# Optimization experiments

Measured on AMD Instinct MI355X. Metric: run time of the kernel, lower is better.

Reference implementation:

```python
import jax, jax.numpy as jnp
import numpy as np

B, S = 4, 2000            # meshes, nodes per mesh
N = B * S                  # total nodes
E = 32000                  # directed edges (before self loops)
H_TR, D_TR, FF, TOUT = 4, 64, 2048, 16
HID, HEADS, HC = 512, 6, 512
DEFORM_IN, NUM_LOOP = 7, 3


def setup_inputs():
    key = jax.random.key(0)
    ks = iter(jax.random.split(key, 64))
    def W(shape):
        return jax.random.normal(next(ks), shape, jnp.float32) / np.sqrt(shape[-1])
    inp = {}
    inp['conv_feat'] = jax.random.normal(next(ks), (B, 1), jnp.float32)
    inp['mesh_feat'] = jax.random.normal(next(ks), (N, 4), jnp.float32)
    inp['x'] = jax.random.normal(next(ks), (N, DEFORM_IN), jnp.float32)
    inp['edge_index'] = jax.random.randint(next(ks), (2, E), 0, N, jnp.int32)
    inp['embed_w'] = W((D_TR, 4)); inp['embed_b'] = jnp.zeros((D_TR,), jnp.float32)
    inp['in_proj_w'] = W((3 * D_TR, D_TR)); inp['in_proj_b'] = jnp.zeros((3 * D_TR,), jnp.float32)
    inp['out_proj_w'] = W((D_TR, D_TR)); inp['out_proj_b'] = jnp.zeros((D_TR,), jnp.float32)
    inp['ln1_g'] = jnp.ones((D_TR,), jnp.float32); inp['ln1_b'] = jnp.zeros((D_TR,), jnp.float32)
    inp['ln2_g'] = jnp.ones((D_TR,), jnp.float32); inp['ln2_b'] = jnp.zeros((D_TR,), jnp.float32)
    inp['ff1_w'] = W((FF, D_TR)); inp['ff1_b'] = jnp.zeros((FF,), jnp.float32)
    inp['ff2_w'] = W((D_TR, FF)); inp['ff2_b'] = jnp.zeros((D_TR,), jnp.float32)
    inp['tout_w'] = W((TOUT, D_TR)); inp['tout_b'] = jnp.zeros((TOUT,), jnp.float32)
    all_feat = DEFORM_IN - 2 + TOUT  # 21
    inp['lin_w'] = W((HID, all_feat)); inp['lin_b'] = jnp.zeros((HID,), jnp.float32)
    gin = 2 + HID  # 514
    inp['gat_wl'] = W((HEADS * HC, gin)); inp['gat_bl'] = jnp.zeros((HEADS * HC,), jnp.float32)
    inp['gat_wr'] = W((HEADS * HC, gin)); inp['gat_br'] = jnp.zeros((HEADS * HC,), jnp.float32)
    inp['gat_att'] = jax.random.normal(next(ks), (HEADS, HC), jnp.float32) / np.sqrt(HC)
    inp['gat_bias'] = jnp.zeros((HC,), jnp.float32)
    inp['coord1_w'] = W((HID // 2, HID)); inp['coord1_b'] = jnp.zeros((HID // 2,), jnp.float32)
    inp['coord2_w'] = W((2, HID // 2)); inp['coord2_b'] = jnp.zeros((2,), jnp.float32)
    return inp


def _ln(h, g, b):
    m = jnp.mean(h, -1, keepdims=True)
    v = jnp.var(h, -1, keepdims=True)
    return (h - m) / jnp.sqrt(v + 1e-5) * g + b


def _mrt_forward(conv_feat, mesh_feat, x, edge_index, embed_w, embed_b, in_proj_w, in_proj_b,
                 out_proj_w, out_proj_b, ln1_g, ln1_b, ln2_g, ln2_b, ff1_w, ff1_b, ff2_w, ff2_b,
                 tout_w, tout_b, lin_w, lin_b, gat_wl, gat_bl, gat_wr, gat_br, gat_att, gat_bias,
                 coord1_w, coord1_b, coord2_w, coord2_b):
    bsz = conv_feat.shape[0]
    feat_dim = mesh_feat.shape[-1]
    # ---- transformer encoder (1 post-norm layer, eval mode => no dropout) ----
    h = mesh_feat.reshape(bsz, -1, feat_dim) @ embed_w.T + embed_b  # [B,S,D]
    qkv = h @ in_proj_w.T + in_proj_b
    q, k, v = jnp.split(qkv, 3, axis=-1)
    dh = D_TR // H_TR
    hd = lambda t: t.reshape(bsz, -1, H_TR, dh)
    attn = jax.nn.softmax(jnp.einsum('bqhd,bkhd->bhqk', hd(q), hd(k)) / np.sqrt(dh), axis=-1)
    o = jnp.einsum('bhqk,bkhd->bqhd', attn, hd(v)).reshape(bsz, -1, D_TR)
    h = _ln(h + (o @ out_proj_w.T + out_proj_b), ln1_g, ln1_b)
    ff = jax.nn.relu(h @ ff1_w.T + ff1_b) @ ff2_w.T + ff2_b
    h = _ln(h + ff, ln2_g, ln2_b)
    feats = (h @ tout_w.T + tout_b).reshape(-1, TOUT)               # [N,16]
    feats = jnp.concatenate([x[:, 2:], feats], axis=1)             # [N,21]
    hidden = jax.nn.selu(feats @ lin_w.T + lin_b)                  # [N,512]
    # ---- recurrent GATv2 deformer loop ----
    coord = x[:, :2]
    n = x.shape[0]
    loops = jnp.arange(n, dtype=edge_index.dtype)                  # self loops (GATv2Conv default)
    src = jnp.concatenate([edge_index[0], loops])
    dst = jnp.concatenate([edge_index[1], loops])
    for _ in range(NUM_LOOP):
        inp = jnp.concatenate([coord, hidden], axis=1)             # [N,514]
        xl = (inp @ gat_wl.T + gat_bl).reshape(n, HEADS, HC)
        xr = (inp @ gat_wr.T + gat_br).reshape(n, HEADS, HC)
        e = jax.nn.leaky_relu(xl[src] + xr[dst], 0.2)              # [Etot,H,C]
        logits = jnp.einsum('ehc,hc->eh', e, gat_att)              # [Etot,H]
        mx = jax.ops.segment_max(logits, dst, num_segments=n)
        a = jnp.exp(logits - mx[dst])
        a = a / jax.ops.segment_sum(a, dst, num_segments=n)[dst]   # softmax per dst node
        agg = jax.ops.segment_sum(xl[src] * a[:, :, None], dst, num_segments=n)  # [N,H,C]
        hidden = jax.nn.selu(jnp.mean(agg, axis=1) + gat_bias)     # concat=False => head mean
        coord = jax.nn.selu(hidden @ coord1_w.T + coord1_b) @ coord2_w.T + coord2_b
    return coord


def reference(conv_feat, mesh_feat, x, edge_index, embed_w, embed_b, in_proj_w, in_proj_b,
              out_proj_w, out_proj_b, ln1_g, ln1_b, ln2_g, ln2_b, ff1_w, ff1_b, ff2_w, ff2_b,
              tout_w, tout_b, lin_w, lin_b, gat_wl, gat_bl, gat_wr, gat_br, gat_att, gat_bias,
              coord1_w, coord1_b, coord2_w, coord2_b):
    return _mrt_forward(conv_feat, mesh_feat, x, edge_index, embed_w, embed_b, in_proj_w, in_proj_b,
                        out_proj_w, out_proj_b, ln1_g, ln1_b, ln2_g, ln2_b, ff1_w, ff1_b, ff2_w, ff2_b,
                        tout_w, tout_b, lin_w, lin_b, gat_wl, gat_bl, gat_wr, gat_br, gat_att, gat_bias,
                        coord1_w, coord1_b, coord2_w, coord2_b)
```

## Files before the change

kernel.cpp:

```cpp
#include <hip/hip_runtime.h>
#include <hip/hip_bf16.h>
#include <math.h>

#define NN     8000
#define MPAD   8064
#define BATCH  4
#define SEQ    2000
#define DTR    64
#define NHTR   4
#define DHD    16
#define FFD    2048
#define TOUTD  16
#define HIDD   512
#define NHEADS 6
#define HCD    512
#define GIND   514
#define GOUT   3072
#define GOUT2  6144
#define NEDGE  32000
#define ELOOP  40000

#define K1     576
#define K2     1152

#define KSPLIT 20
#define KCH    100

#define CDIV(a,b) (((a)+(b)-1)/(b))

using bf16x8 = __attribute__((__ext_vector_type__(8))) __bf16;
using f32x4  = __attribute__((__ext_vector_type__(4))) float;

__device__ __forceinline__ float selu_f(float x){
  const float a = 1.6732632423543772848f;
  const float s = 1.0507009873554805f;
  return x > 0.f ? s * x : s * a * (__expf(x) - 1.f);
}

__device__ __forceinline__ unsigned short f2bf_rn(float x){
  unsigned u = __float_as_uint(x);
  unsigned r = (u + 0x7fffu + ((u >> 16) & 1u)) >> 16;
  return (unsigned short)r;
}
__device__ __forceinline__ float bf2f(unsigned short h){
  return __uint_as_float((unsigned)h << 16);
}

template<int ACT>
__global__ __launch_bounds__(256) void k_gemm(const float* __restrict__ A,
    const float* __restrict__ W, const float* __restrict__ bias,
    float* __restrict__ C, int M, int N, int K)
{
  __shared__ float As[16][68];
  __shared__ float Ws[16][68];
  const int tid = threadIdx.x;
  const int bm = blockIdx.y * 64, bn = blockIdx.x * 64;
  const int tx = tid & 15, ty = tid >> 4;
  float acc[4][4] = {};
  for (int k0 = 0; k0 < K; k0 += 16){
    #pragma unroll
    for (int i = 0; i < 4; ++i){
      int el = tid + (i << 8);
      int kk = el & 15, r = el >> 4;
      int gk = k0 + kk;
      int gm = bm + r;
      As[kk][r] = (gm < M && gk < K) ? A[(size_t)gm * K + gk] : 0.f;
      int gn = bn + r;
      Ws[kk][r] = (gn < N && gk < K) ? W[(size_t)gn * K + gk] : 0.f;
    }
    __syncthreads();
    #pragma unroll
    for (int kk = 0; kk < 16; ++kk){
      float av[4], wv[4];
      #pragma unroll
      for (int i = 0; i < 4; ++i) av[i] = As[kk][ty*4+i];
      #pragma unroll
      for (int j = 0; j < 4; ++j) wv[j] = Ws[kk][tx*4+j];
      #pragma unroll
      for (int i = 0; i < 4; ++i)
        #pragma unroll
        for (int j = 0; j < 4; ++j) acc[i][j] = fmaf(av[i], wv[j], acc[i][j]);
    }
    __syncthreads();
  }
  #pragma unroll
  for (int i = 0; i < 4; ++i){
    int gm = bm + ty*4 + i;
    if (gm >= M) continue;
    #pragma unroll
    for (int j = 0; j < 4; ++j){
      int gn = bn + tx*4 + j;
      if (gn >= N) continue;
      float v = acc[i][j] + bias[gn];
      if (ACT == 1) v = fmaxf(v, 0.f);
      if (ACT == 2) v = selu_f(v);
      C[(size_t)gm * N + gn] = v;
    }
  }
}

__global__ __launch_bounds__(256) void k_gemm_sk(const float* __restrict__ A,
    const float* __restrict__ W, float* __restrict__ part,
    int M, int N, int K, int kchunk)
{
  __shared__ float As[16][68];
  __shared__ float Ws[16][68];
  const int tid = threadIdx.x;
  const int bm = blockIdx.y * 64, bn = blockIdx.x * 64;
  const int kbeg = blockIdx.z * kchunk;
  const int tx = tid & 15, ty = tid >> 4;
  float acc[4][4] = {};
  for (int k0 = kbeg; k0 < kbeg + kchunk; k0 += 16){
    #pragma unroll
    for (int i = 0; i < 4; ++i){
      int el = tid + (i << 8);
      int kk = el & 15, r = el >> 4;
      int gk = k0 + kk;
      int gm = bm + r;
      As[kk][r] = (gm < M && gk < K) ? A[(size_t)gm * K + gk] : 0.f;
      int gn = bn + r;
      Ws[kk][r] = (gn < N && gk < K) ? W[(size_t)gn * K + gk] : 0.f;
    }
    __syncthreads();
    #pragma unroll
    for (int kk = 0; kk < 16; ++kk){
      float av[4], wv[4];
      #pragma unroll
      for (int i = 0; i < 4; ++i) av[i] = As[kk][ty*4+i];
      #pragma unroll
      for (int j = 0; j < 4; ++j) wv[j] = Ws[kk][tx*4+j];
      #pragma unroll
      for (int i = 0; i < 4; ++i)
        #pragma unroll
        for (int j = 0; j < 4; ++j) acc[i][j] = fmaf(av[i], wv[j], acc[i][j]);
    }
    __syncthreads();
  }
  float* pz = part + (size_t)blockIdx.z * M * N;
  #pragma unroll
  for (int i = 0; i < 4; ++i){
    int gm = bm + ty*4 + i;
    if (gm >= M) continue;
    #pragma unroll
    for (int j = 0; j < 4; ++j){
      int gn = bn + tx*4 + j;
      if (gn >= N) continue;
      pz[(size_t)gm * N + gn] = acc[i][j];
    }
  }
}

__global__ __launch_bounds__(256) void k_addln8(const float* __restrict__ x,
    const float* __restrict__ part, const float* __restrict__ bias,
    const float* __restrict__ g, const float* __restrict__ b,
    float* __restrict__ out)
{
  int row = blockIdx.x * 4 + (threadIdx.x >> 6);
  int lane = threadIdx.x & 63;
  if (row >= NN) return;
  float y = bias[lane];
  #pragma unroll
  for (int z = 0; z < 8; ++z) y += part[(size_t)z*NN*DTR + (size_t)row*64 + lane];
  float v = x[(size_t)row*64 + lane] + y;
  float s1 = v, s2 = v * v;
  #pragma unroll
  for (int o = 32; o; o >>= 1){ s1 += __shfl_xor(s1, o); s2 += __shfl_xor(s2, o); }
  float mean = s1 * (1.f/64.f);
  float var  = s2 * (1.f/64.f) - mean * mean;
  float r = rsqrtf(var + 1e-5f);
  out[(size_t)row*64 + lane] = (v - mean) * r * g[lane] + b[lane];
}

__global__ __launch_bounds__(256) void k_coord(const float* __restrict__ part,
    const float* __restrict__ c1b, const float* __restrict__ w2,
    const float* __restrict__ b2, float* __restrict__ out,
    short* __restrict__ abf)
{
  int n = blockIdx.x, t = threadIdx.x;
  float v = c1b[t];
  #pragma unroll
  for (int z = 0; z < 4; ++z) v += part[(size_t)z*NN*256 + (size_t)n*256 + t];
  v = selu_f(v);
  float d0 = v * w2[t], d1 = v * w2[256 + t];
  #pragma unroll
  for (int o = 32; o; o >>= 1){ d0 += __shfl_xor(d0, o); d1 += __shfl_xor(d1, o); }
  __shared__ float red[8];
  int wv = t >> 6;
  if ((t & 63) == 0){ red[wv] = d0; red[4 + wv] = d1; }
  __syncthreads();
  if (t < 2){
    float c = (t == 0 ? red[0]+red[1]+red[2]+red[3] + b2[0]
                      : red[4]+red[5]+red[6]+red[7] + b2[1]);
    out[(size_t)n*2 + t] = c;
    abf[(size_t)n*K2 + t] = (short)f2bf_rn(c);
  }
}

__global__ void k_cvt_w(const float* __restrict__ W, short* __restrict__ Wbf)
{
  int i = blockIdx.x * blockDim.x + threadIdx.x;
  if (i >= GOUT * K1) return;
  int n = i / K1, k = i - K1 * n;
  float v = (k < GIND) ? W[(size_t)n * GIND + k] : 0.f;
  Wbf[i] = (short)f2bf_rn(v);
}

__global__ void k_cvt_a(const float* __restrict__ coord,
                        const float* __restrict__ hidden,
                        short* __restrict__ Abf)
{
  int i = blockIdx.x * blockDim.x + threadIdx.x;
  if (i >= MPAD * K1) return;
  int n = i / K1, k = i - K1 * n;
  float v = 0.f;
  if (n < NN && k < GIND)
    v = (k < 2) ? coord[(size_t)n*2 + k] : hidden[(size_t)n*HIDD + k - 2];
  Abf[(size_t)n * K2 + k] = (short)f2bf_rn(v);
}

__global__ __launch_bounds__(256) void k_gat_mfma(
    const short* __restrict__ Abf, const short* __restrict__ Wbf,
    const float* __restrict__ bl, const float* __restrict__ br,
    unsigned short* __restrict__ Cb)
{
  __shared__ __align__(16) short smem[2 * 128 * 64];
  short* As = smem;
  short* Bs = smem + 128 * 64;
  const int tid  = threadIdx.x;
  int lin = blockIdx.y * 48 + blockIdx.x;
  int xcd = lin & 7;
  int idx = lin >> 3;
  int nb  = xcd * 6 + idx % 6;
  int mb  = idx / 6;
  const int bm = mb * 128, bn = nb * 128;
  const int w    = tid >> 6, lane = tid & 63;
  const int wr   = w >> 1, wc = w & 1;
  const int lrow = lane & 15;

  f32x4 acc[4][4];
  #pragma unroll
  for (int i = 0; i < 4; ++i)
    #pragma unroll
    for (int j = 0; j < 4; ++j) acc[i][j] = (f32x4){0.f, 0.f, 0.f, 0.f};

  for (int kt = 0; kt < 9; ++kt){
    int koff = kt * 64;
    __syncthreads();
    #pragma unroll
    for (int i = 0; i < 4; ++i){
      int l  = i * 256 + tid;
      int r  = l >> 3, j = l & 7;
      int js = j ^ (r & 7);
      const short* ga = Abf + (size_t)(bm + r) * K2 + koff + js * 8;
      const short* gb = Wbf + (size_t)(bn + r) * K1 + koff + js * 8;
      short* la = As + ((i * 256 + w * 64) << 3);
      short* lb = Bs + ((i * 256 + w * 64) << 3);
      __builtin_amdgcn_global_load_lds(
          (const __attribute__((address_space(1))) unsigned*)ga,
          (__attribute__((address_space(3))) unsigned*)la, 16, 0, 0);
      __builtin_amdgcn_global_load_lds(
          (const __attribute__((address_space(1))) unsigned*)gb,
          (__attribute__((address_space(3))) unsigned*)lb, 16, 0, 0);
    }
    __syncthreads();
    #pragma unroll
    for (int ks = 0; ks < 2; ++ks){
      const int co = ((ks * 4 + (lane >> 4)) ^ (lrow & 7)) * 8;
      bf16x8 fa[4], fb[4];
      #pragma unroll
      for (int mi = 0; mi < 4; ++mi)
        fa[mi] = *(const bf16x8*)&As[(wr*64 + mi*16 + lrow) * 64 + co];
      #pragma unroll
      for (int ni = 0; ni < 4; ++ni)
        fb[ni] = *(const bf16x8*)&Bs[(wc*64 + ni*16 + lrow) * 64 + co];
      #pragma unroll
      for (int mi = 0; mi < 4; ++mi)
        #pragma unroll
        for (int ni = 0; ni < 4; ++ni)
          acc[mi][ni] = __builtin_amdgcn_mfma_f32_16x16x32_bf16(
              fa[mi], fb[ni], acc[mi][ni], 0, 0, 0);
    }
  }
  __syncthreads();
  unsigned short* Ct = (unsigned short*)smem;
  #pragma unroll
  for (int mi = 0; mi < 4; ++mi){
    #pragma unroll
    for (int ni = 0; ni < 4; ++ni){
      int col = wc*64 + ni*16 + lrow;
      int gn  = bn + col;
      float bv = (gn < GOUT) ? bl[gn] : br[gn - GOUT];
      #pragma unroll
      for (int j = 0; j < 4; ++j){
        int row  = wr*64 + mi*16 + (lane >> 4)*4 + j;
        int colp = col ^ (((row >> 2) & 3) << 4);
        Ct[row*128 + colp] = f2bf_rn(acc[mi][ni][j] + bv);
      }
    }
  }
  __syncthreads();
  #pragma unroll
  for (int c = 0; c < 8; ++c){
    int g   = c*256 + tid;
    int row = g >> 4, cc = g & 15;
    int ccp = cc ^ (((row >> 2) & 3) << 1);
    int gm  = bm + row;
    if (gm < NN){
      bf16x8 v = *(const bf16x8*)&Ct[row*128 + ccp*8];
      *(bf16x8*)&Cb[(size_t)gm * GOUT2 + bn + cc*8] = v;
    }
  }
}

__global__ void k_embed(const float* __restrict__ mesh,
                        const float* __restrict__ w, const float* __restrict__ b,
                        float* __restrict__ h)
{
  int i = blockIdx.x * blockDim.x + threadIdx.x;
  if (i >= NN * DTR) return;
  int n = i >> 6, d = i & 63;
  const float* mr = mesh + n * 4;
  const float* wr = w + d * 4;
  h[i] = fmaf(mr[0], wr[0], fmaf(mr[1], wr[1], fmaf(mr[2], wr[2], mr[3]*wr[3]))) + b[d];
}

__global__ __launch_bounds__(128) void k_attn_part(const float* __restrict__ qkv,
    float* __restrict__ Pm, float* __restrict__ Pl, float* __restrict__ Pacc)
{
  __shared__ float Ks[KCH][DHD];
  __shared__ float Vs[KCH][DHD];
  const int q1 = blockIdx.x * 128 + threadIdx.x;
  const int q2 = q1 + 1024;
  const int bh = blockIdx.y;
  const int b  = bh >> 2, h = bh & 3;
  const int ks = blockIdx.z;
  const bool v2 = q2 < SEQ;
  const float SC = 0.25f * 1.4426950408889634f;
  float qv1[DHD], qv2[DHD];
  {
    const float4* qr = (const float4*)(qkv + ((size_t)(b*SEQ + q1))*192 + h*DHD);
    #pragma unroll
    for (int j = 0; j < 4; ++j){
      float4 t = qr[j];
      qv1[j*4+0] = t.x; qv1[j*4+1] = t.y; qv1[j*4+2] = t.z; qv1[j*4+3] = t.w;
    }
  }
  if (v2){
    const float4* qr = (const float4*)(qkv + ((size_t)(b*SEQ + q2))*192 + h*DHD);
    #pragma unroll
    for (int j = 0; j < 4; ++j){
      float4 t = qr[j];
      qv2[j*4+0] = t.x; qv2[j*4+1] = t.y; qv2[j*4+2] = t.z; qv2[j*4+3] = t.w;
    }
  } else {
    #pragma unroll
    for (int j = 0; j < DHD; ++j) qv2[j] = 0.f;
  }
  const int kbeg = ks * KCH;
  for (int el = threadIdx.x; el < KCH * 4; el += 128){
    int r = el >> 2, d4 = el & 3;
    const float4* base = (const float4*)(qkv + ((size_t)(b*SEQ + kbeg + r))*192 + h*DHD);
    ((float4*)Ks[r])[d4] = base[16 + d4];
    ((float4*)Vs[r])[d4] = base[32 + d4];
  }
  __syncthreads();
  float m1 = -1e30f, l1 = 0.f, a1[DHD] = {};
  float m2 = -1e30f, l2 = 0.f, a2[DHD] = {};
  for (int r = 0; r < KCH; ++r){
    float s1 = 0.f, s2 = 0.f;
    #pragma unroll
    for (int d = 0; d < DHD; ++d){
      float kd = Ks[r][d];
      s1 = fmaf(qv1[d], kd, s1);
      s2 = fmaf(qv2[d], kd, s2);
    }
    s1 *= SC; s2 *= SC;
    if (__any((s1 > m1 + 8.f) || (s2 > m2 + 8.f))){
      float mn1 = fmaxf(m1, s1), mn2 = fmaxf(m2, s2);
      float c1 = exp2f(m1 - mn1), c2 = exp2f(m2 - mn2);
      l1 *= c1; l2 *= c2;
      #pragma unroll
      for (int d = 0; d < DHD; ++d){ a1[d] *= c1; a2[d] *= c2; }
      m1 = mn1; m2 = mn2;
    }
    float p1 = exp2f(s1 - m1), p2 = exp2f(s2 - m2);
    l1 += p1; l2 += p2;
    #pragma unroll
    for (int d = 0; d < DHD; ++d){
      float vd = Vs[r][d];
      a1[d] = fmaf(p1, vd, a1[d]);
      a2[d] = fmaf(p2, vd, a2[d]);
    }
  }
  {
    size_t qi = ((size_t)bh * SEQ + q1) * KSPLIT + ks;
    Pm[qi] = m1; Pl[qi] = l1;
    #pragma unroll
    for (int d = 0; d < DHD; ++d) Pacc[qi*DHD + d] = a1[d];
  }
  if (v2){
    size_t qi = ((size_t)bh * SEQ + q2) * KSPLIT + ks;
    Pm[qi] = m2; Pl[qi] = l2;
    #pragma unroll
    for (int d = 0; d < DHD; ++d) Pacc[qi*DHD + d] = a2[d];
  }
}

__global__ void k_attn_comb(const float* __restrict__ Pm, const float* __restrict__ Pl,
                            const float* __restrict__ Pacc, float* __restrict__ o)
{
  int qi = blockIdx.x * blockDim.x + threadIdx.x;
  if (qi >= BATCH * NHTR * SEQ) return;
  float m = -1e30f;
  #pragma unroll
  for (int ks = 0; ks < KSPLIT; ++ks) m = fmaxf(m, Pm[(size_t)qi*KSPLIT + ks]);
  float l = 0.f, acc[DHD] = {};
  #pragma unroll
  for (int ks = 0; ks < KSPLIT; ++ks){
    size_t p = (size_t)qi*KSPLIT + ks;
    float sc = exp2f(Pm[p] - m);
    l += Pl[p] * sc;
    #pragma unroll
    for (int d = 0; d < DHD; ++d) acc[d] = fmaf(Pacc[p*DHD + d], sc, acc[d]);
  }
  int bh = qi / SEQ, q = qi - bh * SEQ;
  int b = bh >> 2, h = bh & 3;
  float inv = 1.f / l;
  #pragma unroll
  for (int d = 0; d < DHD; ++d)
    o[((size_t)(b*SEQ + q))*64 + h*DHD + d] = acc[d] * inv;
}

__global__ __launch_bounds__(256) void k_addln(const float* __restrict__ x,
    const float* __restrict__ y, const float* __restrict__ g,
    const float* __restrict__ b, float* __restrict__ out)
{
  int row = blockIdx.x * 4 + (threadIdx.x >> 6);
  int lane = threadIdx.x & 63;
  if (row >= NN) return;
  float v = x[(size_t)row*64 + lane] + y[(size_t)row*64 + lane];
  float s1 = v, s2 = v * v;
  #pragma unroll
  for (int o = 32; o; o >>= 1){ s1 += __shfl_xor(s1, o); s2 += __shfl_xor(s2, o); }
  float mean = s1 * (1.f/64.f);
  float var  = s2 * (1.f/64.f) - mean * mean;
  float r = rsqrtf(var + 1e-5f);
  out[(size_t)row*64 + lane] = (v - mean) * r * g[lane] + b[lane];
}

__global__ void k_concat_feats(const float* __restrict__ x,
                               const float* __restrict__ tout,
                               float* __restrict__ feats)
{
  int i = blockIdx.x * blockDim.x + threadIdx.x;
  if (i >= NN * 21) return;
  int n = i / 21, c = i - 21*n;
  feats[i] = (c < 5) ? x[(size_t)n*7 + 2 + c] : tout[(size_t)n*16 + c - 5];
}

__global__ void k_initcoord(const float* __restrict__ x, float* __restrict__ coord)
{
  int i = blockIdx.x * blockDim.x + threadIdx.x;
  if (i >= NN * 2) return;
  coord[i] = x[(size_t)(i >> 1)*7 + (i & 1)];
}

__global__ void k_count(const int* __restrict__ dst, int* __restrict__ cnt)
{
  int e = blockIdx.x * blockDim.x + threadIdx.x;
  if (e >= ELOOP) return;
  int d = (e < NEDGE) ? dst[e] : e - NEDGE;
  atomicAdd(&cnt[d], 1);
}

__global__ __launch_bounds__(1024) void k_scan(const int* __restrict__ cnt,
                                               int* __restrict__ ptr)
{
  __shared__ int part[1024];
  int tid = threadIdx.x;
  const int per = 8;
  int loc[per]; int s = 0;
  int base = tid * per;
  #pragma unroll
  for (int i = 0; i < per; ++i){
    int v = (base + i < NN) ? cnt[base + i] : 0;
    loc[i] = s; s += v;
  }
  part[tid] = s;
  __syncthreads();
  for (int off = 1; off < 1024; off <<= 1){
    int v = 0;
    if (tid >= off) v = part[tid - off];
    __syncthreads();
    if (tid >= off) part[tid] += v;
    __syncthreads();
  }
  int pre = tid ? part[tid - 1] : 0;
  #pragma unroll
  for (int i = 0; i < per; ++i)
    if (base + i < NN) ptr[base + i] = pre + loc[i];
  if (tid == 1023) ptr[NN] = part[1023];
}

__global__ void k_fill(const int* __restrict__ dst, const int* __restrict__ ptr,
                       int* __restrict__ fil, int* __restrict__ eid)
{
  int e = blockIdx.x * blockDim.x + threadIdx.x;
  if (e >= ELOOP) return;
  int d = (e < NEDGE) ? dst[e] : e - NEDGE;
  int pos = ptr[d] + atomicAdd(&fil[d], 1);
  eid[pos] = e;
}

__global__ __launch_bounds__(256) void k_logits(const unsigned short* __restrict__ xc,
    const int* __restrict__ src_a, const int* __restrict__ dst_a,
    const int* __restrict__ eid, const float* __restrict__ att,
    float* __restrict__ logits2)
{
  int bid = blockIdx.x;
  int wgs = (bid & 7) * 1250 + (bid >> 3);
  int pos = wgs * 4 + (threadIdx.x >> 6);
  if (pos >= ELOOP) return;
  int lane = threadIdx.x & 63;
  int e = eid[pos];
  int s = (e < NEDGE) ? src_a[e] : e - NEDGE;
  int d = (e < NEDGE) ? dst_a[e] : e - NEDGE;
  const uint4* pl = (const uint4*)(xc + (size_t)s * GOUT2);
  const uint4* pr = (const uint4*)(xc + (size_t)d * GOUT2 + GOUT);
  const float4* pa = (const float4*)att;
  #pragma unroll 2
  for (int h = 0; h < NHEADS; ++h){
    uint4 ua = pl[h*64 + lane];
    uint4 ub = pr[h*64 + lane];
    float4 w0 = pa[h*128 + lane*2], w1 = pa[h*128 + lane*2 + 1];
    float acc = 0.f;
    auto pair = [&](unsigned a, unsigned b, float wl, float wh){
      float vl = __uint_as_float(a << 16)        + __uint_as_float(b << 16);
      float vh = __uint_as_float(a & 0xffff0000u)+ __uint_as_float(b & 0xffff0000u);
      vl = vl > 0.f ? vl : 0.2f * vl;
      vh = vh > 0.f ? vh : 0.2f * vh;
      acc = fmaf(vl, wl, acc);
      acc = fmaf(vh, wh, acc);
    };
    pair(ua.x, ub.x, w0.x, w0.y);
    pair(ua.y, ub.y, w0.z, w0.w);
    pair(ua.z, ub.z, w1.x, w1.y);
    pair(ua.w, ub.w, w1.z, w1.w);
    #pragma unroll
    for (int o2 = 32; o2; o2 >>= 1) acc += __shfl_xor(acc, o2);
    if (lane == 0) logits2[pos*NHEADS + h] = acc;
  }
}

__global__ void k_stats(const float* __restrict__ logits2, const int* __restrict__ ptr,
                        float* __restrict__ mx, float* __restrict__ inv)
{
  int i = blockIdx.x * blockDim.x + threadIdx.x;
  if (i >= NN * NHEADS) return;
  int n = i / NHEADS, h = i - NHEADS * n;
  int s0 = ptr[n], s1 = ptr[n + 1];
  float m = -1e30f;
  for (int t = s0; t < s1; ++t) m = fmaxf(m, logits2[t*NHEADS + h]);
  float s = 0.f;
  for (int t = s0; t < s1; ++t) s += __expf(logits2[t*NHEADS + h] - m);
  mx[i] = m; inv[i] = 1.f / s;
}

__global__ __launch_bounds__(256) void k_agg(const unsigned short* __restrict__ xc,
    const float* __restrict__ logits2, const float* __restrict__ mx,
    const float* __restrict__ inv, const int* __restrict__ ptr,
    const int* __restrict__ eid, const int* __restrict__ src_a,
    const float* __restrict__ gbias, float* __restrict__ hidden,
    short* __restrict__ abf)
{
  const int n = blockIdx.x;
  const int tid = threadIdx.x;
  __shared__ float a_sh[64 * NHEADS];
  __shared__ int src_sh[64];
  const int s0 = ptr[n];
  const int deg = ptr[n + 1] - s0;
  float acc[12] = {};
  for (int base = 0; base < deg; base += 64){
    int cnt = min(64, deg - base);
    __syncthreads();
    for (int t = tid; t < cnt * NHEADS; t += 256){
      int ei = t / NHEADS, h = t - NHEADS * ei;
      a_sh[t] = __expf(logits2[(s0 + base + ei)*NHEADS + h] - mx[n*NHEADS + h])
                * inv[n*NHEADS + h];
      if (h == 0){
        int e = eid[s0 + base + ei];
        src_sh[ei] = (e < NEDGE) ? src_a[e] : e - NEDGE;
      }
    }
    __syncthreads();
    for (int i2 = 0; i2 < cnt; ++i2){
      const unsigned* row = (const unsigned*)(xc + (size_t)src_sh[i2] * GOUT2);
      #pragma unroll
      for (int k = 0; k < NHEADS; ++k){
        unsigned u = row[tid + (k << 8)];
        float wgt = a_sh[i2*NHEADS + k];
        acc[2*k]   = fmaf(__uint_as_float(u << 16),         wgt, acc[2*k]);
        acc[2*k+1] = fmaf(__uint_as_float(u & 0xffff0000u), wgt, acc[2*k+1]);
      }
    }
  }
  float m0 = (acc[0]+acc[2]+acc[4]+acc[6]+acc[8]+acc[10]) * (1.f/6.f);
  float m1 = (acc[1]+acc[3]+acc[5]+acc[7]+acc[9]+acc[11]) * (1.f/6.f);
  float2 out;
  out.x = selu_f(m0 + gbias[2*tid]);
  out.y = selu_f(m1 + gbias[2*tid + 1]);
  *(float2*)&hidden[(size_t)n*HIDD + 2*tid] = out;
  unsigned short h0 = f2bf_rn(out.x), h1 = f2bf_rn(out.y);
  *(unsigned*)&abf[(size_t)n*K2 + 2 + 2*tid] = (unsigned)h0 | ((unsigned)h1 << 16);
}

extern "C" void kernel_launch(void* const* d_in, const int* in_sizes, int n_in,
                              void* d_out, int out_size, void* d_ws, size_t ws_size,
                              hipStream_t stream)
{
  const float* mesh     = (const float*)d_in[1];
  const float* xin      = (const float*)d_in[2];
  const int*   ei       = (const int*)d_in[3];
  const float* embed_w  = (const float*)d_in[4];
  const float* embed_b  = (const float*)d_in[5];
  const float* in_proj_w= (const float*)d_in[6];
  const float* in_proj_b= (const float*)d_in[7];
  const float* out_proj_w=(const float*)d_in[8];
  const float* out_proj_b=(const float*)d_in[9];
  const float* ln1_g    = (const float*)d_in[10];
  const float* ln1_b    = (const float*)d_in[11];
  const float* ln2_g    = (const float*)d_in[12];
  const float* ln2_b    = (const float*)d_in[13];
  const float* ff1_w    = (const float*)d_in[14];
  const float* ff1_b    = (const float*)d_in[15];
  const float* ff2_w    = (const float*)d_in[16];
  const float* ff2_b    = (const float*)d_in[17];
  const float* tout_w   = (const float*)d_in[18];
  const float* tout_b   = (const float*)d_in[19];
  const float* lin_w    = (const float*)d_in[20];
  const float* lin_b    = (const float*)d_in[21];
  const float* gat_wl   = (const float*)d_in[22];
  const float* gat_bl   = (const float*)d_in[23];
  const float* gat_wr   = (const float*)d_in[24];
  const float* gat_br   = (const float*)d_in[25];
  const float* gat_att  = (const float*)d_in[26];
  const float* gat_bias = (const float*)d_in[27];
  const float* coord1_w = (const float*)d_in[28];
  const float* coord1_b = (const float*)d_in[29];
  const float* coord2_w = (const float*)d_in[30];
  const float* coord2_b = (const float*)d_in[31];

  const int* esrc = ei;
  const int* edst = ei + NEDGE;

  char* ws = (char*)d_ws;
  size_t off = 0;
  auto alloc = [&](size_t nbytes){
    size_t o = off; off += (nbytes + 255) & ~(size_t)255; return o;
  };
  float* hidden = (float*)(ws + alloc((size_t)NN * HIDD * 4));
  float* coord  = (float*)(ws + alloc((size_t)NN * 2 * 4));
  unsigned short* xc = (unsigned short*)(ws + alloc((size_t)NN * GOUT2 * 2));
  float* logits = (float*)(ws + alloc((size_t)ELOOP * NHEADS * 4));
  float* mxb    = (float*)(ws + alloc((size_t)NN * NHEADS * 4));
  float* invb   = (float*)(ws + alloc((size_t)NN * NHEADS * 4));
  int*   ptr    = (int*)(ws + alloc((size_t)(NN + 1) * 4));
  int*   eid    = (int*)(ws + alloc((size_t)ELOOP * 4));
  int*   cnt    = (int*)(ws + alloc((size_t)NN * 4));
  int*   fil    = (int*)(ws + alloc((size_t)NN * 4));
  short* abf    = (short*)(ws + alloc((size_t)MPAD * K2 * 2));
  short* wlbf   = (short*)(ws + alloc((size_t)GOUT * K1 * 2));
  short* wrbf   = (short*)(ws + alloc((size_t)GOUT * K1 * 2));
  float* part_c1= (float*)(ws + alloc((size_t)4 * NN * 256 * 4));

  char* arena = (char*)xc;
  float* h       = (float*)(arena + ((size_t)0  << 20));
  float* o       = (float*)(arena + ((size_t)2  << 20));
  float* tmp     = (float*)(arena + ((size_t)4  << 20));
  float* feats   = (float*)(arena + ((size_t)6  << 20));
  float* toutb   = (float*)(arena + ((size_t)7  << 20));
  float* qkv     = (float*)(arena + ((size_t)8  << 20));
  float* Pm      = (float*)(arena + ((size_t)15 << 20));
  float* Pl      = (float*)(arena + ((size_t)18 << 20));
  float* Pacc    = (float*)(arena + ((size_t)21 << 20));
  float* part_f2 = (float*)(arena + ((size_t)8  << 20));
  float* ffmid   = (float*)(arena + ((size_t)28 << 20));

  k_embed<<<CDIV(NN*DTR, 256), 256, 0, stream>>>(mesh, embed_w, embed_b, h);
  k_gemm<0><<<dim3(CDIV(192,64), CDIV(NN,64)), 256, 0, stream>>>(h, in_proj_w, in_proj_b, qkv, NN, 192, DTR);
  k_attn_part<<<dim3(CDIV(SEQ,256), BATCH*NHTR, KSPLIT), 128, 0, stream>>>(qkv, Pm, Pl, Pacc);
  k_attn_comb<<<CDIV(BATCH*NHTR*SEQ, 256), 256, 0, stream>>>(Pm, Pl, Pacc, o);
  k_gemm<0><<<dim3(1, CDIV(NN,64)), 256, 0, stream>>>(o, out_proj_w, out_proj_b, tmp, NN, DTR, DTR);
  k_addln<<<CDIV(NN,4), 256, 0, stream>>>(h, tmp, ln1_g, ln1_b, h);
  k_gemm<1><<<dim3(CDIV(FFD,64), CDIV(NN,64)), 256, 0, stream>>>(h, ff1_w, ff1_b, ffmid, NN, FFD, DTR);
  k_gemm_sk<<<dim3(1, CDIV(NN,64), 8), 256, 0, stream>>>(ffmid, ff2_w, part_f2, NN, DTR, FFD, 256);
  k_addln8<<<CDIV(NN,4), 256, 0, stream>>>(h, part_f2, ff2_b, ln2_g, ln2_b, h);
  k_gemm<0><<<dim3(1, CDIV(NN,64)), 256, 0, stream>>>(h, tout_w, tout_b, toutb, NN, TOUTD, DTR);
  k_concat_feats<<<CDIV(NN*21, 256), 256, 0, stream>>>(xin, toutb, feats);
  k_gemm<2><<<dim3(CDIV(HIDD,64), CDIV(NN,64)), 256, 0, stream>>>(feats, lin_w, lin_b, hidden, NN, HIDD, 21);
  k_initcoord<<<CDIV(NN*2, 256), 256, 0, stream>>>(xin, coord);

  hipMemsetAsync(cnt, 0, (size_t)NN * 4, stream);
  hipMemsetAsync(fil, 0, (size_t)NN * 4, stream);
  k_count<<<CDIV(ELOOP, 256), 256, 0, stream>>>(edst, cnt);
  k_scan<<<1, 1024, 0, stream>>>(cnt, ptr);
  k_fill<<<CDIV(ELOOP, 256), 256, 0, stream>>>(edst, ptr, fil, eid);
  k_cvt_w<<<CDIV(GOUT*K1, 256), 256, 0, stream>>>(gat_wl, wlbf);
  k_cvt_w<<<CDIV(GOUT*K1, 256), 256, 0, stream>>>(gat_wr, wrbf);
  k_cvt_a<<<CDIV(MPAD*K1, 256), 256, 0, stream>>>(coord, hidden, abf);

  for (int it = 0; it < 3; ++it){
    k_gat_mfma<<<dim3(48, 63), 256, 0, stream>>>(abf, wlbf, gat_bl, gat_br, xc);
    k_logits<<<ELOOP/4, 256, 0, stream>>>(xc, esrc, edst, eid, gat_att, logits);
    k_stats<<<CDIV(NN*NHEADS, 256), 256, 0, stream>>>(logits, ptr, mxb, invb);
    k_agg<<<NN, 256, 0, stream>>>(xc, logits, mxb, invb, ptr, eid, esrc, gat_bias, hidden, abf);
    k_gemm_sk<<<dim3(CDIV(256,64), CDIV(NN,64), 4), 256, 0, stream>>>(hidden, coord1_w, part_c1, NN, 256, HIDD, 128);
    float* cdst = (it == 2) ? (float*)d_out : coord;
    k_coord<<<NN, 256, 0, stream>>>(part_c1, coord1_b, coord2_w, coord2_b, cdst, abf);
  }
}
```

Baseline: 982.1 us.

## Fold embedding into QKV projection and use naive small-GEMM kernels

```diff
diff --git a/kernel.cpp b/kernel.cpp
--- a/kernel.cpp
+++ b/kernel.cpp
@@ -99,6 +99,23 @@
   }
 }
 
+template<int ACT>
+__global__ void k_gemm_small(const float* __restrict__ A,
+    const float* __restrict__ W, const float* __restrict__ bias,
+    float* __restrict__ C, int M, int N, int K)
+{
+  int i = blockIdx.x * blockDim.x + threadIdx.x;
+  if (i >= M * N) return;
+  int gm = i / N, gn = i - gm * N;
+  const float* ar = A + (size_t)gm * K;
+  const float* wr = W + (size_t)gn * K;
+  float v = bias[gn];
+  for (int k = 0; k < K; ++k) v = fmaf(ar[k], wr[k], v);
+  if (ACT == 1) v = fmaxf(v, 0.f);
+  if (ACT == 2) v = selu_f(v);
+  C[i] = v;
+}
+
 __global__ __launch_bounds__(256) void k_gemm_sk(const float* __restrict__ A,
     const float* __restrict__ W, float* __restrict__ part,
     int M, int N, int K, int kchunk)
@@ -216,6 +233,44 @@
   if (n < NN && k < GIND)
     v = (k < 2) ? coord[(size_t)n*2 + k] : hidden[(size_t)n*HIDD + k - 2];
   Abf[(size_t)n * K2 + k] = (short)f2bf_rn(v);
+}
+
+__global__ void k_wfuse(const float* __restrict__ ipw, const float* __restrict__ ipb,
+                        const float* __restrict__ ew, const float* __restrict__ eb,
+                        float* __restrict__ Wp, float* __restrict__ bp)
+{
+  int c = blockIdx.x * blockDim.x + threadIdx.x;
+  if (c >= 192) return;
+  float w4[4] = {0.f, 0.f, 0.f, 0.f};
+  float bb = 0.f;
+  for (int d = 0; d < 64; ++d){
+    float wq = ipw[c*64 + d];
+    #pragma unroll
+    for (int j = 0; j < 4; ++j) w4[j] = fmaf(wq, ew[d*4 + j], w4[j]);
+    bb = fmaf(wq, eb[d], bb);
+  }
+  #pragma unroll
+  for (int j = 0; j < 4; ++j) Wp[c*4 + j] = w4[j];
+  bp[c] = bb + ipb[c];
+}
+
+__global__ __launch_bounds__(256) void k_embqkv(const float* __restrict__ mesh,
+    const float* __restrict__ ew, const float* __restrict__ eb,
+    const float* __restrict__ Wp, const float* __restrict__ bp,
+    float* __restrict__ h, float* __restrict__ qkv)
+{
+  int n = blockIdx.x, t = threadIdx.x;
+  float m0 = mesh[n*4+0], m1 = mesh[n*4+1], m2 = mesh[n*4+2], m3 = mesh[n*4+3];
+  if (t < 64){
+    const float* wr = ew + t*4;
+    h[(size_t)n*64 + t] =
+      fmaf(m0, wr[0], fmaf(m1, wr[1], fmaf(m2, wr[2], m3*wr[3]))) + eb[t];
+  } else {
+    int c = t - 64;
+    const float* wr = Wp + c*4;
+    qkv[(size_t)n*192 + c] =
+      fmaf(m0, wr[0], fmaf(m1, wr[1], fmaf(m2, wr[2], m3*wr[3]))) + bp[c];
+  }
 }
 
 __global__ __launch_bounds__(256) void k_gat_mfma(
@@ -312,18 +367,6 @@
   }
 }
 
-__global__ void k_embed(const float* __restrict__ mesh,
-                        const float* __restrict__ w, const float* __restrict__ b,
-                        float* __restrict__ h)
-{
-  int i = blockIdx.x * blockDim.x + threadIdx.x;
-  if (i >= NN * DTR) return;
-  int n = i >> 6, d = i & 63;
-  const float* mr = mesh + n * 4;
-  const float* wr = w + d * 4;
-  h[i] = fmaf(mr[0], wr[0], fmaf(mr[1], wr[1], fmaf(mr[2], wr[2], mr[3]*wr[3]))) + b[d];
-}
-
 __global__ __launch_bounds__(128) void k_attn_part(const float* __restrict__ qkv,
     float* __restrict__ Pm, float* __restrict__ Pl, float* __restrict__ Pacc)
 {
@@ -448,21 +491,16 @@
   out[(size_t)row*64 + lane] = (v - mean) * r * g[lane] + b[lane];
 }
 
-__global__ void k_concat_feats(const float* __restrict__ x,
-                               const float* __restrict__ tout,
-                               float* __restrict__ feats)
+__global__ void k_prep(const float* __restrict__ x, const float* __restrict__ tout,
+                       float* __restrict__ feats, float* __restrict__ coord)
 {
   int i = blockIdx.x * blockDim.x + threadIdx.x;
-  if (i >= NN * 21) return;
-  int n = i / 21, c = i - 21*n;
-  feats[i] = (c < 5) ? x[(size_t)n*7 + 2 + c] : tout[(size_t)n*16 + c - 5];
-}
-
-__global__ void k_initcoord(const float* __restrict__ x, float* __restrict__ coord)
-{
-  int i = blockIdx.x * blockDim.x + threadIdx.x;
-  if (i >= NN * 2) return;
-  coord[i] = x[(size_t)(i >> 1)*7 + (i & 1)];
+  if (i >= NN * 23) return;
+  int n = i / 23, c = i - 23*n;
+  if (c < 21)
+    feats[(size_t)n*21 + c] = (c < 5) ? x[(size_t)n*7 + 2 + c] : tout[(size_t)n*16 + c - 5];
+  else
+    coord[(size_t)n*2 + (c - 21)] = x[(size_t)n*7 + (c - 21)];
 }
 
 __global__ void k_count(const int* __restrict__ dst, int* __restrict__ cnt)
@@ -672,6 +710,8 @@
   short* wlbf   = (short*)(ws + alloc((size_t)GOUT * K1 * 2));
   short* wrbf   = (short*)(ws + alloc((size_t)GOUT * K1 * 2));
   float* part_c1= (float*)(ws + alloc((size_t)4 * NN * 256 * 4));
+  float* Wp     = (float*)(ws + alloc((size_t)192 * 4 * 4));
+  float* bp     = (float*)(ws + alloc((size_t)192 * 4));
 
   char* arena = (char*)xc;
   float* h       = (float*)(arena + ((size_t)0  << 20));
@@ -686,19 +726,18 @@
   float* part_f2 = (float*)(arena + ((size_t)8  << 20));
   float* ffmid   = (float*)(arena + ((size_t)28 << 20));
 
-  k_embed<<<CDIV(NN*DTR, 256), 256, 0, stream>>>(mesh, embed_w, embed_b, h);
-  k_gemm<0><<<dim3(CDIV(192,64), CDIV(NN,64)), 256, 0, stream>>>(h, in_proj_w, in_proj_b, qkv, NN, 192, DTR);
+  k_wfuse<<<1, 192, 0, stream>>>(in_proj_w, in_proj_b, embed_w, embed_b, Wp, bp);
+  k_embqkv<<<NN, 256, 0, stream>>>(mesh, embed_w, embed_b, Wp, bp, h, qkv);
   k_attn_part<<<dim3(CDIV(SEQ,256), BATCH*NHTR, KSPLIT), 128, 0, stream>>>(qkv, Pm, Pl, Pacc);
   k_attn_comb<<<CDIV(BATCH*NHTR*SEQ, 256), 256, 0, stream>>>(Pm, Pl, Pacc, o);
-  k_gemm<0><<<dim3(1, CDIV(NN,64)), 256, 0, stream>>>(o, out_proj_w, out_proj_b, tmp, NN, DTR, DTR);
+  k_gemm_small<0><<<CDIV(NN*64, 256), 256, 0, stream>>>(o, out_proj_w, out_proj_b, tmp, NN, 64, 64);
   k_addln<<<CDIV(NN,4), 256, 0, stream>>>(h, tmp, ln1_g, ln1_b, h);
   k_gemm<1><<<dim3(CDIV(FFD,64), CDIV(NN,64)), 256, 0, stream>>>(h, ff1_w, ff1_b, ffmid, NN, FFD, DTR);
   k_gemm_sk<<<dim3(1, CDIV(NN,64), 8), 256, 0, stream>>>(ffmid, ff2_w, part_f2, NN, DTR, FFD, 256);
   k_addln8<<<CDIV(NN,4), 256, 0, stream>>>(h, part_f2, ff2_b, ln2_g, ln2_b, h);
-  k_gemm<0><<<dim3(1, CDIV(NN,64)), 256, 0, stream>>>(h, tout_w, tout_b, toutb, NN, TOUTD, DTR);
-  k_concat_feats<<<CDIV(NN*21, 256), 256, 0, stream>>>(xin, toutb, feats);
-  k_gemm<2><<<dim3(CDIV(HIDD,64), CDIV(NN,64)), 256, 0, stream>>>(feats, lin_w, lin_b, hidden, NN, HIDD, 21);
-  k_initcoord<<<CDIV(NN*2, 256), 256, 0, stream>>>(xin, coord);
+  k_gemm_small<0><<<CDIV(NN*16, 256), 256, 0, stream>>>(h, tout_w, tout_b, toutb, NN, 16, 64);
+  k_prep<<<CDIV(NN*23, 256), 256, 0, stream>>>(xin, toutb, feats, coord);
+  k_gemm_small<2><<<CDIV(NN*512, 256), 256, 0, stream>>>(feats, lin_w, lin_b, hidden, NN, 512, 21);
 
   hipMemsetAsync(cnt, 0, (size_t)NN * 4, stream);
   hipMemsetAsync(fil, 0, (size_t)NN * 4, stream);
```

Measured after the change: 1.099 ms. 12.0% more time.
